# Kernel tuning notes

Measured on AMD Instinct MI355X. Metric: run time of the kernel, lower is better.

Reference implementation:

```python
import jax, jax.numpy as jnp
import numpy as np

STRIDE = 1
PAD = 3
DILATION = 1


def idynamic(x, weight, stride=STRIDE, pad=PAD, dilation=DILATION):
    """Per-pixel dynamic (involution-style) convolution.

    x:      [N, C, H, W]
    weight: [N, G, kh, kw, Ho, Wo]  (per-sample, per-pixel filters, shared across C//G channels)
    out[n,c,h,w] = sum_{kh,kw} weight[n, c//(C//G), kh, kw, h, w] * x[n, c, h_in, w_in]
    with h_in = -pad + h*stride + kh*dilation (zero-padded outside).
    """
    N, C, H, W = x.shape
    _, G, kh, kw, Ho, Wo = weight.shape
    xp = jnp.pad(x, ((0, 0), (0, 0), (pad, pad), (pad, pad)))
    # reshape channels into groups: [N, G, C//G, Hp, Wp]
    xp = xp.reshape(N, G, C // G, H + 2 * pad, W + 2 * pad)
    out = jnp.zeros((N, G, C // G, Ho, Wo), dtype=x.dtype)
    for i in range(kh):          # small fixed kernel-tap loop (unrolled by jit)
        for j in range(kw):
            hi = i * dilation
            wj = j * dilation
            # strided patch: [N, G, C//G, Ho, Wo]
            patch = xp[:, :, :, hi:hi + (Ho - 1) * stride + 1:stride,
                              wj:wj + (Wo - 1) * stride + 1:stride]
            out = out + patch * weight[:, :, i, j][:, :, None, :, :]
    return out.reshape(N, C, Ho, Wo)


def setup_inputs() -> dict:
    key = jax.random.key(0)
    k1, k2 = jax.random.split(key)
    N, C, H, W = 8, 256, 128, 128
    G, KH, KW = 1, 7, 7
    x = jax.random.normal(k1, (N, C, H, W), dtype=jnp.float32)
    weight = jax.random.normal(k2, (N, G, KH, KW, H, W), dtype=jnp.float32)
    return {"x": x, "weight": weight}


def reference(x, weight):
    return idynamic(x, weight)
```

## Files before the change

kernel.cpp:

```cpp
#include <hip/hip_runtime.h>
#include <stdint.h>


#define KH 7
#define KW 7
#define PADC 3
#define HD 128
#define WD 128
#define CD 256
#define TH 8
#define CPB 64
#define PATCH_ROWS 14
#define ROWF 128
#define GUARD 4
#define BUF_FLOATS (GUARD + PATCH_ROWS*ROWF + GUARD)
#define HW (HD*WD)

typedef float f32x4 __attribute__((ext_vector_type(4)));
typedef __attribute__((address_space(3))) float lds_f;

__device__ __forceinline__ void gload_lds16(const float* g, float* l) {
  __builtin_amdgcn_global_load_lds(
      (const __attribute__((address_space(1))) void*)g,
      (__attribute__((address_space(3))) void*)l, 16, 0, 0);
}

#define DS_ISSUE3(P, O0, O1, O2, Q0, Q1, Q2)                        \
  asm volatile("ds_read_b128 %0, %3 offset:" #O0 "\n\t"             \
               "ds_read_b128 %1, %3 offset:" #O1 "\n\t"             \
               "ds_read_b128 %2, %3 offset:" #O2                    \
               : "=&v"(Q0), "=&v"(Q1), "=&v"(Q2) : "v"(P))

#define LGKM_WAIT(N, Q0, Q1, Q2)                                    \
  asm volatile("s_waitcnt lgkmcnt(" #N ")" : "+v"(Q0), "+v"(Q1), "+v"(Q2))

__device__ __forceinline__ float xk(const f32x4 a, const f32x4 b,
                                    const f32x4 c, const int k) {
  return k < 4 ? a[k] : (k < 8 ? b[k - 4] : c[k - 8]);
}

__global__ __launch_bounds__(256, 2)
void dyconv_kernel(const float* __restrict__ x,
                   const float* __restrict__ wt,
                   float* __restrict__ out) {
  __shared__ __align__(16) float lds0[BUF_FLOATS];
  __shared__ __align__(16) float lds1[BUF_FLOATS];

  const int t  = threadIdx.x;
  const int l  = t & 31;
  const int r  = t >> 5;
  const int w0 = l << 2;

  const int bid   = blockIdx.x;
  const int chunk = bid & 3;
  const int strip = (bid >> 2) & 15;
  const int n     = bid >> 6;
  const int h0    = strip * TH;
  const int h     = h0 + r;
  const int c0    = chunk * CPB;

  float wgt[KH][KW][4];
  {
    const float* wb = wt + (size_t)n * (KH*KW) * HW + h * WD + w0;
    #pragma unroll
    for (int i = 0; i < KH; ++i) {
      const int hx = h + i - PADC;
      const bool rowok = (hx >= 0) && (hx < HD);
      #pragma unroll
      for (int j = 0; j < KW; ++j) {
        float4 v = *(const float4*)(wb + (size_t)(i*KW + j) * HW);
        const int xc = w0 + j - PADC;
        wgt[i][j][0] = (rowok && xc+0 >= 0 && xc+0 < WD) ? v.x : 0.f;
        wgt[i][j][1] = (rowok && xc+1 >= 0 && xc+1 < WD) ? v.y : 0.f;
        wgt[i][j][2] = (rowok && xc+2 >= 0 && xc+2 < WD) ? v.z : 0.f;
        wgt[i][j][3] = (rowok && xc+3 >= 0 && xc+3 < WD) ? v.w : 0.f;
      }
    }
  }
  #pragma unroll
  for (int i = 0; i < KH; ++i)
    #pragma unroll
    for (int j = 0; j < KW; ++j)
      #pragma unroll
      for (int p = 0; p < 4; ++p)
        asm volatile("" : "+v"(wgt[i][j][p]));

  if (t < GUARD) {
    lds0[t] = 0.f; lds0[GUARD + PATCH_ROWS*ROWF + t] = 0.f;
    lds1[t] = 0.f; lds1[GUARD + PATCH_ROWS*ROWF + t] = 0.f;
  }

  const int  rrA  = r;
  const int  rrB  = 8 + r;
  const bool hasB = (t < 192);
  const int  hxA  = min(HD-1, max(0, h0 - PADC + rrA));
  const int  hxB  = min(HD-1, max(0, h0 - PADC + rrB));
  const int  srcA = hxA * WD + w0;
  const int  srcB = hxB * WD + w0;
  const int  dstA = GUARD + rrA * ROWF + w0;
  const int  dstB = GUARD + rrB * ROWF + w0;

  const float* xn   = x   + ((size_t)(n * CD + c0)) * HW;
  float*       outp = out + ((size_t)(n * CD + c0)) * HW + h * WD + w0;

  lds_f* P0 = (lds_f*)&lds0[0] + (r * ROWF + (l << 2));
  lds_f* P1 = (lds_f*)&lds1[0] + (r * ROWF + (l << 2));

#define CH_COMPUTE(P)                                                     \
  do {                                                                    \
    f32x4 A0, A1, A2, B0, B1, B2;                                         \
    DS_ISSUE3(P, 0, 16, 32, A0, A1, A2);                                  \
    DS_ISSUE3(P, 512, 528, 544, B0, B1, B2);                              \
    LGKM_WAIT(3, A0, A1, A2); ROW_FMA(0, A0, A1, A2);                     \
    DS_ISSUE3(P, 1024, 1040, 1056, A0, A1, A2);                           \
    LGKM_WAIT(3, B0, B1, B2); ROW_FMA(1, B0, B1, B2);                     \
    DS_ISSUE3(P, 1536, 1552, 1568, B0, B1, B2);                           \
    LGKM_WAIT(3, A0, A1, A2); ROW_FMA(2, A0, A1, A2);                     \
    DS_ISSUE3(P, 2048, 2064, 2080, A0, A1, A2);                           \
    LGKM_WAIT(3, B0, B1, B2); ROW_FMA(3, B0, B1, B2);                     \
    DS_ISSUE3(P, 2560, 2576, 2592, B0, B1, B2);                           \
    LGKM_WAIT(3, A0, A1, A2); ROW_FMA(4, A0, A1, A2);                     \
    DS_ISSUE3(P, 3072, 3088, 3104, A0, A1, A2);                           \
    LGKM_WAIT(3, B0, B1, B2); ROW_FMA(5, B0, B1, B2);                     \
    LGKM_WAIT(0, A0, A1, A2); ROW_FMA(6, A0, A1, A2);                     \
  } while (0)

#define ROW_FMA(I, Q0, Q1, Q2)                                            \
  _Pragma("unroll")                                                       \
  for (int j = 0; j < KW; ++j) {                                          \
    ax += wgt[I][j][0] * xk(Q0, Q1, Q2, j + 1);                           \
    ay += wgt[I][j][1] * xk(Q0, Q1, Q2, j + 2);                           \
    az += wgt[I][j][2] * xk(Q0, Q1, Q2, j + 3);                           \
    aw += wgt[I][j][3] * xk(Q0, Q1, Q2, j + 4);                           \
  }

#define BODY(NXTARR, CURP, CC)                                            \
  do {                                                                    \
    if ((CC) + 1 < CPB) {                                                 \
      const float* xs = xn + ((CC) + 1) * HW;                             \
      gload_lds16(xs + srcA, &NXTARR[dstA]);                              \
      if (hasB) gload_lds16(xs + srcB, &NXTARR[dstB]);                    \
    }                                                                     \
    __builtin_amdgcn_sched_barrier(0);                                    \
    float ax = 0.f, ay = 0.f, az = 0.f, aw = 0.f;                         \
    CH_COMPUTE(CURP);                                                     \
    float4 o; o.x = ax; o.y = ay; o.z = az; o.w = aw;                     \
    *(float4*)(outp + (CC) * HW) = o;                                     \
    asm volatile("s_waitcnt vmcnt(1)" ::: "memory");                      \
    __builtin_amdgcn_s_barrier();                                         \
    __builtin_amdgcn_sched_barrier(0);                                    \
  } while (0)

  gload_lds16(xn + srcA, &lds0[dstA]);
  if (hasB) gload_lds16(xn + srcB, &lds0[dstB]);
  asm volatile("s_waitcnt vmcnt(0) lgkmcnt(0)" ::: "memory");
  __builtin_amdgcn_s_barrier();
  __builtin_amdgcn_sched_barrier(0);

  #pragma unroll 1
  for (int cc = 0; cc < CPB; cc += 2) {
    BODY(lds1, P0, cc);
    BODY(lds0, P1, cc + 1);
  }

#undef CH_COMPUTE
#undef ROW_FMA
#undef BODY
}

extern "C" void kernel_launch(void* const* d_in, const int* in_sizes, int n_in,
                              void* d_out, int out_size, void* d_ws, size_t ws_size,
                              hipStream_t stream) {
  const float* x  = (const float*)d_in[0];
  const float* wt = (const float*)d_in[1];
  float* out      = (float*)d_out;
  hipLaunchKernelGGL(dyconv_kernel, dim3(512), dim3(256), 0, stream, x, wt, out);
}
```

Before: 292.4 us.

## Deepen input prefetch to distance two with a four-slot LDS ring buffer

Replaces the two-buffer LDS ping-pong with a four-slot ring and issues the global-to-LDS copy for channel cc+2 while channel cc is computed. The vmcnt wait is relaxed so that only the oldest staged channel must be complete before the barrier. The goal is to hide more global-load latency behind the per-channel 7x7 FMA work. In exchange, LDS use rises, every thread now loads a second row (two rows of waste per stage), and the launch-bounds occupancy hint drops from 2 to 1.

```diff
diff --git a/kernel.cpp b/kernel.cpp
--- a/kernel.cpp
+++ b/kernel.cpp
@@ -10,10 +10,11 @@
 #define CD 256
 #define TH 8
 #define CPB 64
-#define PATCH_ROWS 14
+#define SROWS 16
 #define ROWF 128
 #define GUARD 4
-#define BUF_FLOATS (GUARD + PATCH_ROWS*ROWF + GUARD)
+#define BUFQ (GUARD + SROWS*ROWF)
+#define NBUF 4
 #define HW (HD*WD)
 
 typedef float f32x4 __attribute__((ext_vector_type(4)));
@@ -39,12 +40,11 @@
   return k < 4 ? a[k] : (k < 8 ? b[k - 4] : c[k - 8]);
 }
 
-__global__ __launch_bounds__(256, 2)
+__global__ __launch_bounds__(256, 1)
 void dyconv_kernel(const float* __restrict__ x,
                    const float* __restrict__ wt,
                    float* __restrict__ out) {
-  __shared__ __align__(16) float lds0[BUF_FLOATS];
-  __shared__ __align__(16) float lds1[BUF_FLOATS];
+  __shared__ __align__(16) float lds4[NBUF][BUFQ];
 
   const int t  = threadIdx.x;
   const int l  = t & 31;
@@ -85,26 +85,38 @@
       for (int p = 0; p < 4; ++p)
         asm volatile("" : "+v"(wgt[i][j][p]));
 
-  if (t < GUARD) {
-    lds0[t] = 0.f; lds0[GUARD + PATCH_ROWS*ROWF + t] = 0.f;
-    lds1[t] = 0.f; lds1[GUARD + PATCH_ROWS*ROWF + t] = 0.f;
-  }
+  if (t < NBUF * GUARD) lds4[t >> 2][t & 3] = 0.f;
 
-  const int  rrA  = r;
-  const int  rrB  = 8 + r;
-  const bool hasB = (t < 192);
-  const int  hxA  = min(HD-1, max(0, h0 - PADC + rrA));
-  const int  hxB  = min(HD-1, max(0, h0 - PADC + rrB));
-  const int  srcA = hxA * WD + w0;
-  const int  srcB = hxB * WD + w0;
-  const int  dstA = GUARD + rrA * ROWF + w0;
-  const int  dstB = GUARD + rrB * ROWF + w0;
+  const int rrA  = r;
+  const int rrB  = 8 + r;
+  const int hxA  = min(HD-1, max(0, h0 - PADC + rrA));
+  const int hxB  = min(HD-1, max(0, h0 - PADC + rrB));
+  const int srcA = hxA * WD + w0;
+  const int srcB = hxB * WD + w0;
+  const int dstA = GUARD + rrA * ROWF + w0;
+  const int dstB = GUARD + rrB * ROWF + w0;
 
   const float* xn   = x   + ((size_t)(n * CD + c0)) * HW;
   float*       outp = out + ((size_t)(n * CD + c0)) * HW + h * WD + w0;
 
-  lds_f* P0 = (lds_f*)&lds0[0] + (r * ROWF + (l << 2));
-  lds_f* P1 = (lds_f*)&lds1[0] + (r * ROWF + (l << 2));
+  lds_f* Pb = (lds_f*)&lds4[0][0] + (r * ROWF + (l << 2));
+
+#define STAGE2(C)                                                         \
+  do {                                                                    \
+    const float* xs = xn + (size_t)(C) * HW;                              \
+    float* B = &lds4[(C) & 3][0];                                         \
+    gload_lds16(xs + srcA, B + dstA);                                     \
+    gload_lds16(xs + srcB, B + dstB);                                     \
+  } while (0)
+
+#define ROW_FMA(I, Q0, Q1, Q2)                                            \
+  _Pragma("unroll")                                                       \
+  for (int j = 0; j < KW; ++j) {                                          \
+    ax += wgt[I][j][0] * xk(Q0, Q1, Q2, j + 1);                           \
+    ay += wgt[I][j][1] * xk(Q0, Q1, Q2, j + 2);                           \
+    az += wgt[I][j][2] * xk(Q0, Q1, Q2, j + 3);                           \
+    aw += wgt[I][j][3] * xk(Q0, Q1, Q2, j + 4);                           \
+  }
 
 #define CH_COMPUTE(P)                                                     \
   do {                                                                    \
@@ -125,47 +137,40 @@
     LGKM_WAIT(0, A0, A1, A2); ROW_FMA(6, A0, A1, A2);                     \
   } while (0)
 
-#define ROW_FMA(I, Q0, Q1, Q2)                                            \
-  _Pragma("unroll")                                                       \
-  for (int j = 0; j < KW; ++j) {                                          \
-    ax += wgt[I][j][0] * xk(Q0, Q1, Q2, j + 1);                           \
-    ay += wgt[I][j][1] * xk(Q0, Q1, Q2, j + 2);                           \
-    az += wgt[I][j][2] * xk(Q0, Q1, Q2, j + 3);                           \
-    aw += wgt[I][j][3] * xk(Q0, Q1, Q2, j + 4);                           \
-  }
-
-#define BODY(NXTARR, CURP, CC)                                            \
+#define COMPUTE_STORE(CC)                                                 \
   do {                                                                    \
-    if ((CC) + 1 < CPB) {                                                 \
-      const float* xs = xn + ((CC) + 1) * HW;                             \
-      gload_lds16(xs + srcA, &NXTARR[dstA]);                              \
-      if (hasB) gload_lds16(xs + srcB, &NXTARR[dstB]);                    \
-    }                                                                     \
-    __builtin_amdgcn_sched_barrier(0);                                    \
+    lds_f* P = Pb + ((CC) & 3) * BUFQ;                                    \
     float ax = 0.f, ay = 0.f, az = 0.f, aw = 0.f;                         \
-    CH_COMPUTE(CURP);                                                     \
+    CH_COMPUTE(P);                                                        \
     float4 o; o.x = ax; o.y = ay; o.z = az; o.w = aw;                     \
-    *(float4*)(outp + (CC) * HW) = o;                                     \
-    asm volatile("s_waitcnt vmcnt(1)" ::: "memory");                      \
-    __builtin_amdgcn_s_barrier();                                         \
-    __builtin_amdgcn_sched_barrier(0);                                    \
+    *(float4*)(outp + (size_t)(CC) * HW) = o;                             \
   } while (0)
 
-  gload_lds16(xn + srcA, &lds0[dstA]);
-  if (hasB) gload_lds16(xn + srcB, &lds0[dstB]);
+  STAGE2(0);
+  STAGE2(1);
   asm volatile("s_waitcnt vmcnt(0) lgkmcnt(0)" ::: "memory");
   __builtin_amdgcn_s_barrier();
   __builtin_amdgcn_sched_barrier(0);
 
   #pragma unroll 1
-  for (int cc = 0; cc < CPB; cc += 2) {
-    BODY(lds1, P0, cc);
-    BODY(lds0, P1, cc + 1);
+  for (int cc = 0; cc < CPB - 2; ++cc) {
+    STAGE2(cc + 2);
+    __builtin_amdgcn_sched_barrier(0);
+    COMPUTE_STORE(cc);
+    asm volatile("s_waitcnt vmcnt(4)" ::: "memory");
+    __builtin_amdgcn_s_barrier();
+    __builtin_amdgcn_sched_barrier(0);
   }
+  COMPUTE_STORE(CPB - 2);
+  asm volatile("s_waitcnt vmcnt(2)" ::: "memory");
+  __builtin_amdgcn_s_barrier();
+  __builtin_amdgcn_sched_barrier(0);
+  COMPUTE_STORE(CPB - 1);
 
+#undef STAGE2
+#undef ROW_FMA
 #undef CH_COMPUTE
-#undef ROW_FMA
-#undef BODY
+#undef COMPUTE_STORE
 }
 
 extern "C" void kernel_launch(void* const* d_in, const int* in_sizes, int n_in,
```

New measurement: 269.6 us. 1.08x faster.
